# Kernel tuning notes

Measured on AMD Instinct MI355X. Metric: run time of the kernel, lower is better.

The kernel has to match this reference:

```python
import jax, jax.numpy as jnp
import numpy as np

HID = 2048
HEADS = 16
HEAD_DIM = HID // HEADS  # 128
MLP_HID = 4 * HID
L_IMG = 2048
L_TXT = 256


def _layernorm(x, eps=1e-6):
    mu = jnp.mean(x, axis=-1, keepdims=True)
    xc = x - mu
    var = jnp.mean(xc * xc, axis=-1, keepdims=True)
    return xc * jax.lax.rsqrt(var + eps)


def _rmsnorm(x, scale, eps=1e-6):
    xf = x.astype(jnp.float32)
    rrms = jax.lax.rsqrt(jnp.mean(xf * xf, axis=-1, keepdims=True) + eps)
    return (xf * rrms).astype(x.dtype) * scale


def _apply_rope(x, pe):
    # x: [B,H,L,D], pe: [1,1,L,D/2,2,2]
    B, H, L, D = x.shape
    xf = x.astype(jnp.float32).reshape(B, H, L, D // 2, 1, 2)
    out = pe[..., 0] * xf[..., 0] + pe[..., 1] * xf[..., 1]  # [B,H,L,D/2,2]
    return out.reshape(B, H, L, D).astype(x.dtype)


def _attention(q, k, v, pe):
    q = _apply_rope(q, pe)
    k = _apply_rope(k, pe)
    scale = 1.0 / jnp.sqrt(jnp.float32(q.shape[-1])).astype(q.dtype)
    logits = jnp.einsum('bhqd,bhkd->bhqk', q, k) * scale
    probs = jax.nn.softmax(logits, axis=-1)
    out = jnp.einsum('bhqk,bhkd->bhqd', probs, v)
    B, H, L, D = out.shape
    return out.transpose(0, 2, 1, 3).reshape(B, L, H * D)


def _modulation(vec, w, b):
    out = jnp.dot(jax.nn.silu(vec), w) + b  # [B, 6*dim]
    return jnp.split(out[:, None, :], 6, axis=-1)


def _qkv_heads(x, w, b):
    B, L, _ = x.shape
    qkv = (jnp.dot(x, w) + b).reshape(B, L, 3, HEADS, HEAD_DIM)
    qkv = qkv.transpose(2, 0, 3, 1, 4)  # [3,B,H,L,D]
    return qkv[0], qkv[1], qkv[2]


def _mlp(x, w1, b1, w2, b2):
    return jnp.dot(jax.nn.gelu(jnp.dot(x, w1) + b1, approximate=True), w2) + b2


def setup_inputs() -> dict:
    key = jax.random.key(0)
    ks = iter(jax.random.split(key, 32))
    s = 0.02
    d = {
        'img': jax.random.normal(next(ks), (1, L_IMG, HID), jnp.float32),
        'txt': jax.random.normal(next(ks), (1, L_TXT, HID), jnp.float32),
        'vec': jax.random.normal(next(ks), (1, HID), jnp.float32),
        'pe': jax.random.normal(next(ks), (1, 1, L_TXT + L_IMG, HEAD_DIM // 2, 2, 2), jnp.float32),
    }
    for p in ('img', 'txt'):
        d[p + '_mod_w'] = jax.random.normal(next(ks), (HID, 6 * HID), jnp.float32) * s
        d[p + '_mod_b'] = jnp.zeros((6 * HID,), jnp.float32)
        d[p + '_qkv_w'] = jax.random.normal(next(ks), (HID, 3 * HID), jnp.float32) * s
        d[p + '_qkv_b'] = jnp.zeros((3 * HID,), jnp.float32)
        d[p + '_q_scale'] = jnp.ones((HEAD_DIM,), jnp.float32)
        d[p + '_k_scale'] = jnp.ones((HEAD_DIM,), jnp.float32)
        d[p + '_proj_w'] = jax.random.normal(next(ks), (HID, HID), jnp.float32) * s
        d[p + '_proj_b'] = jnp.zeros((HID,), jnp.float32)
        d[p + '_mlp_w1'] = jax.random.normal(next(ks), (HID, MLP_HID), jnp.float32) * s
        d[p + '_mlp_b1'] = jnp.zeros((MLP_HID,), jnp.float32)
        d[p + '_mlp_w2'] = jax.random.normal(next(ks), (MLP_HID, HID), jnp.float32) * s
        d[p + '_mlp_b2'] = jnp.zeros((HID,), jnp.float32)
    return d


def reference(img, txt, vec, pe,
              img_mod_w, img_mod_b, img_qkv_w, img_qkv_b, img_q_scale, img_k_scale,
              img_proj_w, img_proj_b, img_mlp_w1, img_mlp_b1, img_mlp_w2, img_mlp_b2,
              txt_mod_w, txt_mod_b, txt_qkv_w, txt_qkv_b, txt_q_scale, txt_k_scale,
              txt_proj_w, txt_proj_b, txt_mlp_w1, txt_mlp_b1, txt_mlp_w2, txt_mlp_b2):
    i_sh1, i_sc1, i_g1, i_sh2, i_sc2, i_g2 = _modulation(vec, img_mod_w, img_mod_b)
    t_sh1, t_sc1, t_g1, t_sh2, t_sc2, t_g2 = _modulation(vec, txt_mod_w, txt_mod_b)

    img_modulated = (1 + i_sc1) * _layernorm(img) + i_sh1
    iq, ik, iv = _qkv_heads(img_modulated, img_qkv_w, img_qkv_b)
    iq = _rmsnorm(iq, img_q_scale)
    ik = _rmsnorm(ik, img_k_scale)

    txt_modulated = (1 + t_sc1) * _layernorm(txt) + t_sh1
    tq, tk, tv = _qkv_heads(txt_modulated, txt_qkv_w, txt_qkv_b)
    tq = _rmsnorm(tq, txt_q_scale)
    tk = _rmsnorm(tk, txt_k_scale)

    q = jnp.concatenate((tq, iq), axis=2)
    k = jnp.concatenate((tk, ik), axis=2)
    v = jnp.concatenate((tv, iv), axis=2)
    attn = _attention(q, k, v, pe)  # [B, L_txt+L_img, HID]
    Lt = txt.shape[1]
    txt_attn, img_attn = attn[:, :Lt], attn[:, Lt:]

    img = img + i_g1 * (jnp.dot(img_attn, img_proj_w) + img_proj_b)
    img = img + i_g2 * _mlp((1 + i_sc2) * _layernorm(img) + i_sh2,
                            img_mlp_w1, img_mlp_b1, img_mlp_w2, img_mlp_b2)

    txt = txt + t_g1 * (jnp.dot(txt_attn, txt_proj_w) + txt_proj_b)
    txt = txt + t_g2 * _mlp((1 + t_sc2) * _layernorm(txt) + t_sh2,
                            txt_mlp_w1, txt_mlp_b1, txt_mlp_w2, txt_mlp_b2)
    return img, txt
```

## Files before the change

### kernel.cpp

```cpp
#include <hip/hip_runtime.h>
#include <math.h>

typedef unsigned short u16;
typedef short bf16x8 __attribute__((ext_vector_type(8)));
typedef float f32x4 __attribute__((ext_vector_type(4)));

#define HID 2048
#define NH 16
#define HD 128
#define LI 2048
#define LT 256
#define LA 2304
#define MODW 12288

__device__ __forceinline__ u16 f2bf(float f) {
  unsigned int u = __float_as_uint(f);
  u += 0x7fff + ((u >> 16) & 1);
  return (u16)(u >> 16);
}
__device__ __forceinline__ float bf2f(u16 b) {
  return __uint_as_float(((unsigned int)b) << 16);
}

__device__ __forceinline__ void gload16(const void* g, void* l) {
  __builtin_amdgcn_global_load_lds(
      (const __attribute__((address_space(1))) unsigned int*)g,
      (__attribute__((address_space(3))) unsigned int*)l, 16, 0, 0);
}

__global__ void k_mod_partial(const float* __restrict__ vec,
                              const float* __restrict__ wi,
                              const float* __restrict__ wt,
                              float* __restrict__ part) {
  __shared__ float sv[256];
  int j = blockIdx.x * 256 + threadIdx.x;
  int k0 = blockIdx.y * 256;
  const float* w = blockIdx.z ? wt : wi;
  float v = vec[k0 + threadIdx.x];
  sv[threadIdx.x] = v / (1.f + expf(-v));
  __syncthreads();
  float acc = 0.f;
  for (int kk = 0; kk < 256; ++kk)
    acc += sv[kk] * w[(size_t)(k0 + kk) * MODW + j];
  part[(size_t)(blockIdx.z * 8 + blockIdx.y) * MODW + j] = acc;
}

__global__ void k_mod_reduce(const float* __restrict__ part,
                             const float* __restrict__ bi,
                             const float* __restrict__ bt,
                             float* __restrict__ mod) {
  int i = blockIdx.x * 256 + threadIdx.x;
  int s = i / MODW, j = i % MODW;
  const float* b = s ? bt : bi;
  float v = b[j];
#pragma unroll
  for (int c = 0; c < 8; ++c) v += part[(size_t)(s * 8 + c) * MODW + j];
  mod[i] = v;
}

__global__ void k_ln_mod(const float* __restrict__ xi, const float* __restrict__ xt,
                         const float* __restrict__ shi, const float* __restrict__ sci,
                         const float* __restrict__ sht, const float* __restrict__ sct,
                         u16* __restrict__ out) {
  int r = blockIdx.x;
  bool txs = r < LT;
  const float* xr = txs ? (xt + (size_t)r * HID) : (xi + (size_t)(r - LT) * HID);
  const float* sh = txs ? sht : shi;
  const float* sc = txs ? sct : sci;
  float4 v0 = ((const float4*)xr)[threadIdx.x * 2];
  float4 v1 = ((const float4*)xr)[threadIdx.x * 2 + 1];
  float s1 = v0.x + v0.y + v0.z + v0.w + v1.x + v1.y + v1.z + v1.w;
  float s2 = v0.x * v0.x + v0.y * v0.y + v0.z * v0.z + v0.w * v0.w +
             v1.x * v1.x + v1.y * v1.y + v1.z * v1.z + v1.w * v1.w;
#pragma unroll
  for (int m = 1; m < 64; m <<= 1) { s1 += __shfl_xor(s1, m); s2 += __shfl_xor(s2, m); }
  __shared__ float red[8];
  int wid = threadIdx.x >> 6;
  if ((threadIdx.x & 63) == 0) { red[wid] = s1; red[4 + wid] = s2; }
  __syncthreads();
  float tot  = red[0] + red[1] + red[2] + red[3];
  float tot2 = red[4] + red[5] + red[6] + red[7];
  float mu = tot * (1.f / HID);
  float var = tot2 * (1.f / HID) - mu * mu;
  float rs = rsqrtf(var + 1e-6f);
  int c = threadIdx.x * 8;
  float v[8] = {v0.x, v0.y, v0.z, v0.w, v1.x, v1.y, v1.z, v1.w};
  u16 o[8] __attribute__((aligned(16)));
#pragma unroll
  for (int u = 0; u < 8; ++u)
    o[u] = f2bf((v[u] - mu) * rs * (1.f + sc[c + u]) + sh[c + u]);
  *(uint4*)&out[(size_t)r * HID + c] = *(uint4*)o;
}

__global__ void k_tconv(const float* __restrict__ src, u16* __restrict__ dst,
                        int K, int N) {
  __shared__ __align__(16) float t[64][65];
  int n0 = blockIdx.x * 64, k0 = blockIdx.y * 64;
  int tr = threadIdx.x >> 4;
  int tc = (threadIdx.x & 15) * 4;
#pragma unroll
  for (int i = 0; i < 4; ++i) {
    int r = i * 16 + tr;
    float4 v = *(const float4*)&src[(size_t)(k0 + r) * N + n0 + tc];
    t[r][tc] = v.x; t[r][tc + 1] = v.y; t[r][tc + 2] = v.z; t[r][tc + 3] = v.w;
  }
  __syncthreads();
#pragma unroll
  for (int i = 0; i < 4; ++i) {
    int nr = i * 16 + tr;
    ushort4 o;
    o.x = f2bf(t[tc][nr]); o.y = f2bf(t[tc + 1][nr]);
    o.z = f2bf(t[tc + 2][nr]); o.w = f2bf(t[tc + 3][nr]);
    *(ushort4*)&dst[(size_t)(n0 + nr) * K + k0 + tc] = o;
  }
}

template<int MODE>
__global__ __launch_bounds__(256, 4) void k_gemm(
    const u16* __restrict__ A, int lda,
    const u16* __restrict__ B0, const u16* __restrict__ B1, int ldb,
    void* __restrict__ out0, void* __restrict__ out1, int ldc,
    const float* __restrict__ b0, const float* __restrict__ b1, int K,
    const float* __restrict__ x0, const float* __restrict__ x1,
    const float* __restrict__ g0, const float* __restrict__ g1,
    u16* __restrict__ part) {
  __shared__ __align__(16) u16 lA[128 * 64];
  __shared__ __align__(16) u16 lB[128 * 64];
  int gx = gridDim.x, nwg = gx * gridDim.y;
  int bid = blockIdx.y * gx + blockIdx.x;
  int sw = (bid & 7) * (nwg >> 3) + (bid >> 3);
  int by = sw / gx, bx = sw - by * gx;
  int m0 = by * 128, n0 = bx * 128;
  bool txs = (m0 < LT);
  const u16* Bt = txs ? B1 : B0;
  const float* bias = txs ? b1 : b0;
  int mr = txs ? m0 : m0 - LT;
  int z = blockIdx.z;
  int Kh = K / (int)gridDim.z;
  int tid = threadIdx.x, lane = tid & 63, wid = tid >> 6;
  int wh = wid >> 1, ww = wid & 1;
  f32x4 acc[4][4] = {};
  const char* Ab = (const char*)(A + (size_t)m0 * lda + (size_t)z * Kh);
  const char* Bb = (const char*)(Bt + (size_t)n0 * ldb + (size_t)z * Kh);
  int ko = (lane >> 4) * 8, cl = lane & 15;
  for (int k0 = 0; k0 < Kh; k0 += 64) {
#pragma unroll
    for (int i = 0; i < 4; ++i) {
      int o = (i * 256 + tid) * 16;
      int r = o >> 7, cb = o & 127;
      gload16(Ab + (size_t)r * (lda * 2) + k0 * 2 + cb, (char*)lA + o);
      gload16(Bb + (size_t)r * (ldb * 2) + k0 * 2 + cb, (char*)lB + o);
    }
    __syncthreads();
#pragma unroll
    for (int kk = 0; kk < 64; kk += 32) {
      bf16x8 a[4], b[4];
#pragma unroll
      for (int m = 0; m < 4; ++m)
        a[m] = *(const bf16x8*)&lA[(wh * 64 + m * 16 + cl) * 64 + kk + ko];
#pragma unroll
      for (int n = 0; n < 4; ++n)
        b[n] = *(const bf16x8*)&lB[(ww * 64 + n * 16 + cl) * 64 + kk + ko];
#pragma unroll
      for (int m = 0; m < 4; ++m)
#pragma unroll
        for (int n = 0; n < 4; ++n)
          acc[m][n] = __builtin_amdgcn_mfma_f32_16x16x32_bf16(a[m], b[n], acc[m][n], 0, 0, 0);
    }
    __syncthreads();
  }
  int rg = (lane >> 4) * 4;
#pragma unroll
  for (int m = 0; m < 4; ++m) {
    int r0 = wh * 64 + m * 16 + rg;
#pragma unroll
    for (int n = 0; n < 4; ++n) {
      int gcol = n0 + ww * 64 + n * 16 + cl;
#pragma unroll
      for (int j = 0; j < 4; ++j) {
        float v = acc[m][n][j];
        if (MODE == 3) {
          part[(size_t)z * (LA * (size_t)HID) + (size_t)(m0 + r0 + j) * ldc + gcol] = f2bf(v);
        } else {
          v += bias[gcol];
          size_t orow = (size_t)(mr + r0 + j);
          if (MODE == 0) {
            ((float*)(txs ? out1 : out0))[orow * ldc + gcol] = v;
          } else if (MODE == 4) {
            ((u16*)(txs ? out1 : out0))[orow * ldc + gcol] = f2bf(v);
          } else if (MODE == 1) {
            float z2 = 1.5957691216057308f * (v + 0.044715f * v * v * v);
            ((u16*)(txs ? out1 : out0))[orow * ldc + gcol] =
                f2bf(v / (1.f + __expf(-z2)));
          } else {
            const float* xin = txs ? x1 : x0;
            const float* g = txs ? g1 : g0;
            ((float*)(txs ? out1 : out0))[orow * ldc + gcol] =
                xin[orow * ldc + gcol] + g[gcol] * v;
          }
        }
      }
    }
  }
}

__global__ void k_red2(const u16* __restrict__ P,
                       const float* __restrict__ bias0, const float* __restrict__ bias1,
                       const float* __restrict__ g0, const float* __restrict__ g1,
                       const float* __restrict__ xi, const float* __restrict__ xt,
                       float* __restrict__ oimg, float* __restrict__ otxt) {
  size_t i = ((size_t)blockIdx.x * 256 + threadIdx.x) * 4;
  const size_t S = (size_t)LA * HID;
  int row = (int)(i >> 11), col = (int)(i & (HID - 1));
  ushort4 a0 = *(const ushort4*)&P[i];
  ushort4 a1 = *(const ushort4*)&P[i + S];
  bool txs = row < LT;
  const float* bias = txs ? bias1 : bias0;
  const float* g = txs ? g1 : g0;
  size_t off = txs ? (size_t)row * HID + col : (size_t)(row - LT) * HID + col;
  const float* xin = (txs ? xt : xi) + off;
  float* out = (txs ? otxt : oimg) + off;
  float4 x = *(const float4*)xin;
  float4 o;
  o.x = x.x + g[col] * (bf2f(a0.x) + bf2f(a1.x) + bias[col]);
  o.y = x.y + g[col + 1] * (bf2f(a0.y) + bf2f(a1.y) + bias[col + 1]);
  o.z = x.z + g[col + 2] * (bf2f(a0.z) + bf2f(a1.z) + bias[col + 2]);
  o.w = x.w + g[col + 3] * (bf2f(a0.w) + bf2f(a1.w) + bias[col + 3]);
  *(float4*)out = o;
}

__global__ void k_qkv_post(const u16* __restrict__ qkv,
                           const float* __restrict__ qsi, const float* __restrict__ ksi,
                           const float* __restrict__ qst, const float* __restrict__ kst,
                           const float* __restrict__ pe,
                           u16* __restrict__ Q, u16* __restrict__ K, u16* __restrict__ V) {
  int h = blockIdx.x, lg = blockIdx.y, lane = threadIdx.x;
  bool txs = lg < LT;
  const float* qs = txs ? qst : qsi;
  const float* ks = txs ? kst : ksi;
  const u16* base = qkv + (size_t)lg * 6144 + h * HD;
  float q0 = bf2f(base[2 * lane]), q1 = bf2f(base[2 * lane + 1]);
  float k0 = bf2f(base[2048 + 2 * lane]), k1 = bf2f(base[2048 + 2 * lane + 1]);
  float v0 = bf2f(base[4096 + 2 * lane]), v1 = bf2f(base[4096 + 2 * lane + 1]);
  float sq = q0 * q0 + q1 * q1, sk = k0 * k0 + k1 * k1;
#pragma unroll
  for (int m = 1; m < 64; m <<= 1) { sq += __shfl_xor(sq, m); sk += __shfl_xor(sk, m); }
  float rq = rsqrtf(sq * (1.f / HD) + 1e-6f), rk = rsqrtf(sk * (1.f / HD) + 1e-6f);
  q0 *= rq * qs[2 * lane]; q1 *= rq * qs[2 * lane + 1];
  k0 *= rk * ks[2 * lane]; k1 *= rk * ks[2 * lane + 1];
  float4 p = *(const float4*)&pe[(size_t)lg * 256 + lane * 4];
  float qa = p.x * q0 + p.y * q1, qb = p.z * q0 + p.w * q1;
  float ka = p.x * k0 + p.y * k1, kb = p.z * k0 + p.w * k1;
  size_t ob = ((size_t)h * LA + lg) * HD + 2 * lane;
  Q[ob] = f2bf(qa); Q[ob + 1] = f2bf(qb);
  K[ob] = f2bf(ka); K[ob + 1] = f2bf(kb);
  V[ob] = f2bf(v0); V[ob + 1] = f2bf(v1);
}

__global__ void k_vtrans(const u16* __restrict__ V, u16* __restrict__ Vt) {
  __shared__ __align__(16) u16 t[64][72];
  int l0 = blockIdx.x * 64, d0 = blockIdx.y * 64, h = blockIdx.z;
  const u16* src = V + (size_t)h * LA * HD;
#pragma unroll
  for (int jj = 0; jj < 2; ++jj) {
    int idx = (jj * 256 + threadIdx.x) * 8;
    int r = idx >> 6, c = idx & 63;
    *(uint4*)&t[r][c] = *(const uint4*)&src[(size_t)(l0 + r) * HD + d0 + c];
  }
  __syncthreads();
  u16* dst = Vt + (size_t)h * HD * LA;
#pragma unroll
  for (int jj = 0; jj < 2; ++jj) {
    int idx = (jj * 256 + threadIdx.x) * 8;
    int r = idx >> 6, c = idx & 63;
    u16 o[8] __attribute__((aligned(16)));
#pragma unroll
    for (int u = 0; u < 8; ++u) o[u] = t[c + u][r];
    *(uint4*)&dst[(size_t)(d0 + r) * LA + l0 + c] = *(uint4*)o;
  }
}

__global__ __launch_bounds__(576) void k_flash(
    const u16* __restrict__ Q, const u16* __restrict__ Kg,
    const u16* __restrict__ Vt, u16* __restrict__ attn) {
  __shared__ __align__(16) u16 Ks[2][64 * 128];
  __shared__ __align__(16) u16 Vs[2][128 * 64];
  __shared__ __align__(16) u16 Ps[9][16 * 64];
  int h = blockIdx.y, q0 = blockIdx.x * 144;
  int tid = threadIdx.x, lane = tid & 63, w = tid >> 6;
  int ko = (lane >> 4) * 8, cl = lane & 15;
  const char* Kb = (const char*)(Kg + (size_t)h * LA * HD);
  const char* Vb = (const char*)(Vt + (size_t)h * HD * LA);
  bf16x8 qf[4];
  {
    const u16* Qr = Q + ((size_t)h * LA + q0 + w * 16 + cl) * HD;
#pragma unroll
    for (int kk = 0; kk < 4; ++kk) qf[kk] = *(const bf16x8*)&Qr[kk * 32 + ko];
  }
  f32x4 oacc[8] = {};
  float mst[4] = {-1e30f, -1e30f, -1e30f, -1e30f};
  float lst[4] = {0.f, 0.f, 0.f, 0.f};

  auto stage = [&](int t0, int buf) {
    if (tid < 512) {
#pragma unroll
      for (int i = 0; i < 2; ++i) {
        int o = (i * 512 + tid) * 16;
        int r = o >> 8, c = o & 255;
        gload16(Kb + (size_t)(t0 + r) * 256 + (c ^ ((r & 7) << 4)),
                (char*)Ks[buf] + o);
        int r2 = o >> 7, c2 = o & 127;
        gload16(Vb + (size_t)r2 * (LA * 2) + (size_t)t0 * 2 + (c2 ^ ((r2 & 7) << 4)),
                (char*)Vs[buf] + o);
      }
    }
  };

  stage(0, 0);
  __syncthreads();
  for (int t = 0; t < LA / 64; ++t) {
    int buf = t & 1;
    if (t < LA / 64 - 1) stage((t + 1) * 64, buf ^ 1);
    f32x4 sacc[4] = {};
    __builtin_amdgcn_s_setprio(1);
#pragma unroll
    for (int kk = 0; kk < 4; ++kk) {
      int cb = (kk * 32 + ko) * 2;
#pragma unroll
      for (int n = 0; n < 4; ++n) {
        int row = n * 16 + cl;
        bf16x8 bk = *(const bf16x8*)&Ks[buf][row * 128 + ((cb ^ ((row & 7) << 4)) >> 1)];
        sacc[n] = __builtin_amdgcn_mfma_f32_16x16x32_bf16(qf[kk], bk, sacc[n], 0, 0, 0);
      }
    }
    __builtin_amdgcn_s_setprio(0);
    const float scale = 0.08838834764831845f;
    float mx[4];
#pragma unroll
    for (int j = 0; j < 4; ++j) {
      float m1 = -1e30f;
#pragma unroll
      for (int n = 0; n < 4; ++n) { sacc[n][j] *= scale; m1 = fmaxf(m1, sacc[n][j]); }
#pragma unroll
      for (int m = 1; m < 16; m <<= 1) m1 = fmaxf(m1, __shfl_xor(m1, m));
      mx[j] = m1;
    }
    float dmax = fmaxf(fmaxf(mx[0] - mst[0], mx[1] - mst[1]),
                       fmaxf(mx[2] - mst[2], mx[3] - mst[3]));
    if (!__all(dmax <= 8.f)) {
#pragma unroll
      for (int j = 0; j < 4; ++j) {
        float mnew = fmaxf(mst[j], mx[j]);
        float alpha = __expf(mst[j] - mnew);
        lst[j] *= alpha; mst[j] = mnew;
#pragma unroll
        for (int nd = 0; nd < 8; ++nd) oacc[nd][j] *= alpha;
      }
    }
    float p[4][4];
#pragma unroll
    for (int j = 0; j < 4; ++j) {
      float s = 0.f;
#pragma unroll
      for (int n = 0; n < 4; ++n) { p[n][j] = __expf(sacc[n][j] - mst[j]); s += p[n][j]; }
#pragma unroll
      for (int m = 1; m < 16; m <<= 1) s += __shfl_xor(s, m);
      lst[j] += s;
    }
#pragma unroll
    for (int j = 0; j < 4; ++j) {
      int pr = (lane >> 4) * 4 + j;
#pragma unroll
      for (int n = 0; n < 4; ++n)
        Ps[w][pr * 64 + ((((n * 16 + cl) * 2) ^ ((pr & 7) << 4)) >> 1)] = f2bf(p[n][j]);
    }
    __builtin_amdgcn_s_setprio(1);
#pragma unroll
    for (int kk = 0; kk < 64; kk += 32) {
      int cb = (kk + ko) * 2;
      bf16x8 ap = *(const bf16x8*)&Ps[w][cl * 64 + ((cb ^ ((cl & 7) << 4)) >> 1)];
#pragma unroll
      for (int nd = 0; nd < 8; ++nd) {
        int vr = nd * 16 + cl;
        bf16x8 bv = *(const bf16x8*)&Vs[buf][vr * 64 + ((cb ^ ((vr & 7) << 4)) >> 1)];
        oacc[nd] = __builtin_amdgcn_mfma_f32_16x16x32_bf16(ap, bv, oacc[nd], 0, 0, 0);
      }
    }
    __builtin_amdgcn_s_setprio(0);
    __syncthreads();
  }
#pragma unroll
  for (int j = 0; j < 4; ++j) {
    int lrow = q0 + w * 16 + (lane >> 4) * 4 + j;
    float inv = 1.f / lst[j];
#pragma unroll
    for (int nd = 0; nd < 8; ++nd)
      attn[(size_t)lrow * HID + h * HD + nd * 16 + cl] = f2bf(oacc[nd][j] * inv);
  }
}

extern "C" void kernel_launch(void* const* d_in, const int* in_sizes, int n_in,
                              void* d_out, int out_size, void* d_ws, size_t ws_size,
                              hipStream_t stream) {
  const float* img = (const float*)d_in[0];
  const float* txt = (const float*)d_in[1];
  const float* vec = (const float*)d_in[2];
  const float* pe  = (const float*)d_in[3];
  const float* imod_w = (const float*)d_in[4];
  const float* imod_b = (const float*)d_in[5];
  const float* iqkv_w = (const float*)d_in[6];
  const float* iqkv_b = (const float*)d_in[7];
  const float* iq_s   = (const float*)d_in[8];
  const float* ik_s   = (const float*)d_in[9];
  const float* iproj_w = (const float*)d_in[10];
  const float* iproj_b = (const float*)d_in[11];
  const float* imlp_w1 = (const float*)d_in[12];
  const float* imlp_b1 = (const float*)d_in[13];
  const float* imlp_w2 = (const float*)d_in[14];
  const float* imlp_b2 = (const float*)d_in[15];
  const float* tmod_w = (const float*)d_in[16];
  const float* tmod_b = (const float*)d_in[17];
  const float* tqkv_w = (const float*)d_in[18];
  const float* tqkv_b = (const float*)d_in[19];
  const float* tq_s   = (const float*)d_in[20];
  const float* tk_s   = (const float*)d_in[21];
  const float* tproj_w = (const float*)d_in[22];
  const float* tproj_b = (const float*)d_in[23];
  const float* tmlp_w1 = (const float*)d_in[24];
  const float* tmlp_b1 = (const float*)d_in[25];
  const float* tmlp_w2 = (const float*)d_in[26];
  const float* tmlp_b2 = (const float*)d_in[27];
  (void)in_sizes; (void)n_in; (void)out_size; (void)ws_size;

  float* oimg = (float*)d_out;
  float* otxt = oimg + (size_t)LI * HID;

  char* p = (char*)d_ws;
  auto alloc = [&](size_t b) { char* r = p; p += (b + 255) & ~(size_t)255; return r; };
  float* part = (float*)alloc((size_t)16 * MODW * 4);
  float* mod  = (float*)alloc((size_t)2 * MODW * 4);
  u16*  xm    = (u16*)alloc((size_t)LA * HID * 2);
  u16*  wt_i  = (u16*)alloc((size_t)8192 * 2048 * 2);
  u16*  wt_t  = (u16*)alloc((size_t)8192 * 2048 * 2);
  u16*  qkvr  = (u16*)alloc((size_t)LA * 6144 * 2);
  u16*  Qb    = (u16*)alloc((size_t)NH * LA * HD * 2);
  u16*  Kb    = (u16*)alloc((size_t)NH * LA * HD * 2);
  u16*  Vb    = (u16*)alloc((size_t)NH * LA * HD * 2);
  u16*  Vtb   = (u16*)alloc((size_t)NH * LA * HD * 2);
  u16*  attn  = (u16*)alloc((size_t)LA * HID * 2);
  u16*  hb    = (u16*)alloc((size_t)LA * 8192 * 2);
  u16*  kpart = (u16*)alloc((size_t)2 * LA * HID * 2);

  const float* MI = mod;
  const float* MT = mod + MODW;

  k_mod_partial<<<dim3(48, 8, 2), 256, 0, stream>>>(vec, imod_w, tmod_w, part);
  k_mod_reduce<<<dim3(96), 256, 0, stream>>>(part, imod_b, tmod_b, mod);

  k_ln_mod<<<dim3(LA), 256, 0, stream>>>(img, txt, MI, MI + 2048, MT, MT + 2048, xm);

  k_tconv<<<dim3(96, 32), 256, 0, stream>>>(iqkv_w, wt_i, 2048, 6144);
  k_tconv<<<dim3(96, 32), 256, 0, stream>>>(tqkv_w, wt_t, 2048, 6144);
  k_gemm<4><<<dim3(48, 18), 256, 0, stream>>>(xm, 2048, wt_i, wt_t, 2048,
      qkvr + (size_t)LT * 6144, qkvr, 6144, iqkv_b, tqkv_b, 2048,
      nullptr, nullptr, nullptr, nullptr, nullptr);

  k_qkv_post<<<dim3(NH, LA), 64, 0, stream>>>(qkvr, iq_s, ik_s, tq_s, tk_s, pe, Qb, Kb, Vb);
  k_vtrans<<<dim3(36, 2, NH), 256, 0, stream>>>(Vb, Vtb);

  k_flash<<<dim3(16, NH), 576, 0, stream>>>(Qb, Kb, Vtb, attn);

  k_tconv<<<dim3(32, 32), 256, 0, stream>>>(iproj_w, wt_i, 2048, 2048);
  k_tconv<<<dim3(32, 32), 256, 0, stream>>>(tproj_w, wt_t, 2048, 2048);
  k_gemm<2><<<dim3(16, 18), 256, 0, stream>>>(attn, 2048, wt_i, wt_t, 2048,
      oimg, otxt, 2048, iproj_b, tproj_b, 2048,
      img, txt, MI + 4096, MT + 4096, nullptr);

  k_ln_mod<<<dim3(LA), 256, 0, stream>>>(oimg, otxt, MI + 6144, MI + 8192,
                                         MT + 6144, MT + 8192, xm);

  k_tconv<<<dim3(128, 32), 256, 0, stream>>>(imlp_w1, wt_i, 2048, 8192);
  k_tconv<<<dim3(128, 32), 256, 0, stream>>>(tmlp_w1, wt_t, 2048, 8192);
  k_gemm<1><<<dim3(64, 18), 256, 0, stream>>>(xm, 2048, wt_i, wt_t, 2048,
      hb + (size_t)LT * 8192, hb, 8192, imlp_b1, tmlp_b1, 2048,
      nullptr, nullptr, nullptr, nullptr, nullptr);

  k_tconv<<<dim3(32, 128), 256, 0, stream>>>(imlp_w2, wt_i, 8192, 2048);
  k_tconv<<<dim3(32, 128), 256, 0, stream>>>(tmlp_w2, wt_t, 8192, 2048);
  k_gemm<3><<<dim3(16, 18, 2), 256, 0, stream>>>(hb, 8192, wt_i, wt_t, 8192,
      nullptr, nullptr, 2048, nullptr, nullptr, 8192,
      nullptr, nullptr, nullptr, nullptr, kpart);
  k_red2<<<dim3(4608), 256, 0, stream>>>(kpart, imlp_b2, tmlp_b2,
      MI + 10240, MT + 10240, oimg, otxt, oimg, otxt);
}
```

Measured before the change: 679.7 us.

## Remap GEMM and flash blocks per XCD and merge paired weight conversions

Rewrites the GEMM block-index swizzle so each of the 8 XCDs owns a contiguous range of N-columns, with the split-K index folded into the mapping. The flash kernel is remapped so each XCD handles two whole heads, keeping K/V reuse inside one XCD's L2. The img and txt weight-transpose/convert launches are also merged into a single launch using blockIdx.z. The goal is better L2 locality on the chiplet design and fewer kernel launches. The new mappings assume grid x is divisible by 8 and a fixed 16x16 flash grid.

```diff
diff --git a/kernel.cpp b/kernel.cpp
--- a/kernel.cpp
+++ b/kernel.cpp
@@ -92,9 +92,12 @@
   *(uint4*)&out[(size_t)r * HID + c] = *(uint4*)o;
 }
 
-__global__ void k_tconv(const float* __restrict__ src, u16* __restrict__ dst,
+__global__ void k_tconv(const float* __restrict__ srcI, const float* __restrict__ srcT,
+                        u16* __restrict__ dstI, u16* __restrict__ dstT,
                         int K, int N) {
   __shared__ __align__(16) float t[64][65];
+  const float* src = blockIdx.z ? srcT : srcI;
+  u16* dst = blockIdx.z ? dstT : dstI;
   int n0 = blockIdx.x * 64, k0 = blockIdx.y * 64;
   int tr = threadIdx.x >> 4;
   int tc = (threadIdx.x & 15) * 4;
@@ -126,17 +129,20 @@
     u16* __restrict__ part) {
   __shared__ __align__(16) u16 lA[128 * 64];
   __shared__ __align__(16) u16 lB[128 * 64];
-  int gx = gridDim.x, nwg = gx * gridDim.y;
-  int bid = blockIdx.y * gx + blockIdx.x;
-  int sw = (bid & 7) * (nwg >> 3) + (bid >> 3);
-  int by = sw / gx, bx = sw - by * gx;
+  int gx = gridDim.x, gy = gridDim.y, gz = gridDim.z;
+  int bid = ((int)blockIdx.z * gy + blockIdx.y) * gx + blockIdx.x;
+  int nbxl = gx >> 3;
+  int xcd = bid & 7, j0 = bid >> 3;
+  int by = j0 % gy;
+  int u = j0 / gy;
+  int z = u % gz;
+  int bx = xcd * nbxl + u / gz;
   int m0 = by * 128, n0 = bx * 128;
   bool txs = (m0 < LT);
   const u16* Bt = txs ? B1 : B0;
   const float* bias = txs ? b1 : b0;
   int mr = txs ? m0 : m0 - LT;
-  int z = blockIdx.z;
-  int Kh = K / (int)gridDim.z;
+  int Kh = K / gz;
   int tid = threadIdx.x, lane = tid & 63, wid = tid >> 6;
   int wh = wid >> 1, ww = wid & 1;
   f32x4 acc[4][4] = {};
@@ -286,7 +292,10 @@
   __shared__ __align__(16) u16 Ks[2][64 * 128];
   __shared__ __align__(16) u16 Vs[2][128 * 64];
   __shared__ __align__(16) u16 Ps[9][16 * 64];
-  int h = blockIdx.y, q0 = blockIdx.x * 144;
+  int bid = blockIdx.y * gridDim.x + blockIdx.x;
+  int xcd = bid & 7, j0 = bid >> 3;
+  int h = xcd * 2 + (j0 >> 4);
+  int q0 = (j0 & 15) * 144;
   int tid = threadIdx.x, lane = tid & 63, w = tid >> 6;
   int ko = (lane >> 4) * 8, cl = lane & 15;
   const char* Kb = (const char*)(Kg + (size_t)h * LA * HD);
@@ -459,8 +468,7 @@
 
   k_ln_mod<<<dim3(LA), 256, 0, stream>>>(img, txt, MI, MI + 2048, MT, MT + 2048, xm);
 
-  k_tconv<<<dim3(96, 32), 256, 0, stream>>>(iqkv_w, wt_i, 2048, 6144);
-  k_tconv<<<dim3(96, 32), 256, 0, stream>>>(tqkv_w, wt_t, 2048, 6144);
+  k_tconv<<<dim3(96, 32, 2), 256, 0, stream>>>(iqkv_w, tqkv_w, wt_i, wt_t, 2048, 6144);
   k_gemm<4><<<dim3(48, 18), 256, 0, stream>>>(xm, 2048, wt_i, wt_t, 2048,
       qkvr + (size_t)LT * 6144, qkvr, 6144, iqkv_b, tqkv_b, 2048,
       nullptr, nullptr, nullptr, nullptr, nullptr);
@@ -470,8 +478,7 @@
 
   k_flash<<<dim3(16, NH), 576, 0, stream>>>(Qb, Kb, Vtb, attn);
 
-  k_tconv<<<dim3(32, 32), 256, 0, stream>>>(iproj_w, wt_i, 2048, 2048);
-  k_tconv<<<dim3(32, 32), 256, 0, stream>>>(tproj_w, wt_t, 2048, 2048);
+  k_tconv<<<dim3(32, 32, 2), 256, 0, stream>>>(iproj_w, tproj_w, wt_i, wt_t, 2048, 2048);
   k_gemm<2><<<dim3(16, 18), 256, 0, stream>>>(attn, 2048, wt_i, wt_t, 2048,
       oimg, otxt, 2048, iproj_b, tproj_b, 2048,
       img, txt, MI + 4096, MT + 4096, nullptr);
@@ -479,14 +486,12 @@
   k_ln_mod<<<dim3(LA), 256, 0, stream>>>(oimg, otxt, MI + 6144, MI + 8192,
                                          MT + 6144, MT + 8192, xm);
 
-  k_tconv<<<dim3(128, 32), 256, 0, stream>>>(imlp_w1, wt_i, 2048, 8192);
-  k_tconv<<<dim3(128, 32), 256, 0, stream>>>(tmlp_w1, wt_t, 2048, 8192);
+  k_tconv<<<dim3(128, 32, 2), 256, 0, stream>>>(imlp_w1, tmlp_w1, wt_i, wt_t, 2048, 8192);
   k_gemm<1><<<dim3(64, 18), 256, 0, stream>>>(xm, 2048, wt_i, wt_t, 2048,
       hb + (size_t)LT * 8192, hb, 8192, imlp_b1, tmlp_b1, 2048,
       nullptr, nullptr, nullptr, nullptr, nullptr);
 
-  k_tconv<<<dim3(32, 128), 256, 0, stream>>>(imlp_w2, wt_i, 8192, 2048);
-  k_tconv<<<dim3(32, 128), 256, 0, stream>>>(tmlp_w2, wt_t, 8192, 2048);
+  k_tconv<<<dim3(32, 128, 2), 256, 0, stream>>>(imlp_w2, tmlp_w2, wt_i, wt_t, 8192, 2048);
   k_gemm<3><<<dim3(16, 18, 2), 256, 0, stream>>>(hb, 8192, wt_i, wt_t, 8192,
       nullptr, nullptr, 2048, nullptr, nullptr, 8192,
       nullptr, nullptr, nullptr, nullptr, kpart);
```

New measurement: 661.5 us. 1.03x faster.
